# Performance work log

Hardware: AMD Instinct MI355X
Metric: run time of the kernel (lower is better)

The kernel has to match this reference:

```python
import jax, jax.numpy as jnp
import numpy as np

H = 8
DA, DP, DK = 2048, 1024, 1024
B, N = 4, 2048
DOUT = 512
INNER = (DA + DP + DK) // H  # 512 = heads*dim_head


def setup_inputs() -> dict:
    key = jax.random.key(0)
    ks = jax.random.split(key, 7)
    x = jax.random.normal(ks[0], (B, N, DA + DP + DK), jnp.float32)
    mask = jax.random.randint(ks[1], (B, 1, N, N), 0, 2, jnp.int32)
    W_a = jax.random.normal(ks[2], (3 * DA // H, DA), jnp.float32) * (DA ** -0.5)
    W_p = jax.random.normal(ks[3], (3 * DP // H, DP), jnp.float32) * (DP ** -0.5)
    W_k = jax.random.normal(ks[4], (3 * DK // H, DK), jnp.float32) * (DK ** -0.5)
    W_out = jax.random.normal(ks[5], (DOUT, INNER), jnp.float32) * (INNER ** -0.5)
    b_out = jnp.zeros((DOUT,), jnp.float32)
    return {"x": x, "W_a": W_a, "W_p": W_p, "W_k": W_k,
            "W_out": W_out, "b_out": b_out, "mask": mask}


def _heads(t):  # [b, n, h*d] -> [b, h, n, d]
    b, n, hd = t.shape
    return t.reshape(b, n, H, hd // H).transpose(0, 2, 1, 3)


def reference(x, W_a, W_p, W_k, W_out, b_out, mask):
    # three branch QKV projections (each branch sees its own slice of x)
    qkv_a = x[..., :DA] @ W_a.T                      # [b, n, 3*DA/H]
    qkv_p = x[..., DA:DA + DP] @ W_p.T               # [b, n, 3*DP/H]
    qkv_k = x[..., DA + DP:] @ W_k.T                 # [b, n, 3*DK/H]
    q_a, k_a, v_a = [_heads(t) for t in jnp.split(qkv_a, 3, axis=-1)]
    q_p, k_p, v_p = [_heads(t) for t in jnp.split(qkv_p, 3, axis=-1)]
    q_k, k_k, v_k = [_heads(t) for t in jnp.split(qkv_k, 3, axis=-1)]

    m = mask > 0                                     # [b, 1, n, n]
    neg = jnp.asarray(-1e10, x.dtype)

    def branch(q, k, d):
        dots = jnp.einsum('bhid,bhjd->bhij', q, k) * (d ** -0.5)
        return jax.nn.softmax(jnp.where(m, dots, neg), axis=-1)

    # betas = [1,1,1] normalized -> 1/3 each (the nn.Parameters are unused in fwd)
    attn = (branch(q_a, k_a, DA) + branch(q_p, k_p, DP) + branch(q_k, k_k, DK)) / 3.0

    v = jnp.concatenate([v_a, v_p, v_k], axis=-1)    # [b, h, n, INNER/H]
    out = jnp.einsum('bhij,bhjd->bhid', attn, v)     # [b, h, n, INNER/H]
    out = out.transpose(0, 2, 1, 3).reshape(x.shape[0], x.shape[1], INNER)
    return out @ W_out.T + b_out
```

## Files before the change

kernel.cpp:

```cpp
#include <hip/hip_runtime.h>
#include <hip/hip_bf16.h>

typedef __attribute__((ext_vector_type(8))) __bf16 bf16x8;
typedef __attribute__((ext_vector_type(4))) float f32x4;
typedef unsigned short u16;
typedef unsigned int u32;
typedef unsigned long long u64;

__device__ __forceinline__ u32 cvtpk(float lo, float hi) {
  u32 r;
  asm("v_cvt_pk_bf16_f32 %0, %1, %2" : "=v"(r) : "v"(lo), "v"(hi));
  return r;
}
__device__ __forceinline__ float rexp2(float x) {
  float r;
  asm("v_exp_f32 %0, %1" : "=v"(r) : "v"(x));
  return r;
}
__device__ __forceinline__ void gl_lds16(const void* g, void* l) {
  __builtin_amdgcn_global_load_lds((const __attribute__((address_space(1))) void*)g,
                                   (__attribute__((address_space(3))) void*)l, 16, 0, 0);
}

__global__ __launch_bounds__(256) void prep_kernel(
    const float* __restrict__ x, u16* __restrict__ xb,
    const float* __restrict__ Wa, const float* __restrict__ Wp,
    const float* __restrict__ Wk, const float* __restrict__ Wo,
    u16* __restrict__ Wab, u16* __restrict__ Wpb,
    u16* __restrict__ Wkb, u16* __restrict__ Wob,
    const int* __restrict__ mask, u64* __restrict__ bits, int xblocks) {
  int bid = blockIdx.x;
  if (bid < xblocks) {
    const int idx = (bid * 256 + threadIdx.x) * 16;
    const float4 a0 = *(const float4*)(x + idx);
    const float4 a1 = *(const float4*)(x + idx + 4);
    const float4 a2 = *(const float4*)(x + idx + 8);
    const float4 a3 = *(const float4*)(x + idx + 12);
    uint4 t0, t1;
    t0.x = cvtpk(a0.x, a0.y); t0.y = cvtpk(a0.z, a0.w);
    t0.z = cvtpk(a1.x, a1.y); t0.w = cvtpk(a1.z, a1.w);
    t1.x = cvtpk(a2.x, a2.y); t1.y = cvtpk(a2.z, a2.w);
    t1.z = cvtpk(a3.x, a3.y); t1.w = cvtpk(a3.z, a3.w);
    *(uint4*)(xb + idx) = t0;
    *(uint4*)(xb + idx + 8) = t1;
    return;
  }
  bid -= xblocks;
  if (bid < 2560) {
    const float* s; u16* d; int base;
    if (bid < 1536)      { s = Wa; d = Wab; base = bid; }
    else if (bid < 1920) { s = Wp; d = Wpb; base = bid - 1536; }
    else if (bid < 2304) { s = Wk; d = Wkb; base = bid - 1920; }
    else                 { s = Wo; d = Wob; base = bid - 2304; }
    const int idx = (base * 256 + threadIdx.x) * 4;
    const float4 v = *(const float4*)(s + idx);
    *(uint2*)(d + idx) = make_uint2(cvtpk(v.x, v.y), cvtpk(v.z, v.w));
    return;
  }
  bid -= 2560;
  const int lane = threadIdx.x & 63;
  const long long gw = (long long)bid * 4 + (threadIdx.x >> 6);
  const long long nwaves = 1024LL * 4;
  const long long nwords = 16777216LL / 64;
  for (long long i = gw; i < nwords; i += nwaves) {
    const int m = mask[i * 64 + lane];
    const u64 bal = __ballot(m > 0);
    if (lane == 0) bits[i] = bal;
  }
}

__device__ __forceinline__ void qkv_store(
    float v0, float v1, float v2, float v3, int m_base, int c,
    int dhs, int seg, float fs,
    u16* __restrict__ Qb, u16* __restrict__ Kb, u16* __restrict__ Vt) {
  const int which = c >> (3 + dhs);
  const float f = (which == 0) ? fs : 1.0f;
  const u32 r01 = cvtpk(v0 * f, v1 * f);
  const u32 r23 = cvtpk(v2 * f, v3 * f);
  const u16 bvv[4] = {(u16)r01, (u16)(r01 >> 16), (u16)r23, (u16)(r23 >> 16)};
  const int hd_mask = (8 << dhs) - 1;
  const int r = c & hd_mask;
  const int hh = r >> dhs;
  const int d = r & ((1 << dhs) - 1);
  #pragma unroll
  for (int j = 0; j < 4; ++j) {
    const int m = m_base + j;
    const int bb = m >> 11, n = m & 2047;
    const size_t bhn = (size_t)(bb * 8 + hh) * 2048 + n;
    const u16 bv = bvv[j];
    if (which == 0)      Qb[bhn * 64 + seg + d] = bv;
    else if (which == 1) Kb[bhn * 64 + seg + d] = bv;
    else {
      const int nk6 = n & 63;
      const int pos = ((nk6 >> 5) << 5) | (((nk6 & 15) >> 2) << 3)
                    | ((nk6 & 3) << 1) | ((nk6 >> 4) & 1);
      Vt[((size_t)(bb * 8 + hh) * 64 + seg + d) * 2048 + (n & ~63) + pos] = bv;
    }
  }
}

__global__ __launch_bounds__(256) void qkv_gemm_kernel(
    const u16* __restrict__ xb, const u16* __restrict__ Wa,
    const u16* __restrict__ Wp, const u16* __restrict__ Wk,
    u16* __restrict__ Qb, u16* __restrict__ Kb, u16* __restrict__ Vt) {
  __shared__ u16 lA[64 * 64];
  __shared__ u16 lB[128 * 64];

  const int tid = threadIdx.x;
  const int w = tid >> 6, l = tid & 63;
  const int lr = l & 15, lg = l >> 4;

  const int wg = blockIdx.x;
  const int xcd = wg & 7;
  const int q = wg >> 3;
  const int mtl = q / 12, nt = q % 12;
  const int mt = (xcd << 4) + mtl;

  const u16* W; int xoff, Kd, col0, dhs, seg;
  if (nt < 6)      { W = Wa; xoff = 0;    Kd = 2048; col0 = nt * 128;       dhs = 5; seg = 0;  }
  else if (nt < 9) { W = Wp; xoff = 2048; Kd = 1024; col0 = (nt - 6) * 128; dhs = 4; seg = 32; }
  else             { W = Wk; xoff = 3072; Kd = 1024; col0 = (nt - 9) * 128; dhs = 4; seg = 48; }
  const float qscale = (dhs == 5) ? 0.031880107f : 0.045084220f;

  const int m0 = mt * 64;
  f32x4 acc[4][2] = {};
  const int ubase = tid & ~63;

  const int nk = Kd >> 6;
  #pragma unroll 1
  for (int kt = 0; kt < nk; ++kt) {
    const int k0 = kt << 6;
    #pragma unroll
    for (int i = 0; i < 2; ++i) {
      const int ch = i * 256 + tid;
      const int row = ch >> 3, c8 = (ch & 7) << 3;
      gl_lds16(xb + (size_t)(m0 + row) * 4096 + xoff + k0 + c8,
               lA + (size_t)(i * 256 + ubase) * 8);
    }
    #pragma unroll
    for (int i = 0; i < 4; ++i) {
      const int ch = i * 256 + tid;
      const int row = ch >> 3, c8 = (ch & 7) << 3;
      gl_lds16(W + (size_t)(col0 + row) * Kd + k0 + c8,
               lB + (size_t)(i * 256 + ubase) * 8);
    }
    __syncthreads();
    bf16x8 af[4][2], bfr[2][2];
    #pragma unroll
    for (int mi = 0; mi < 4; ++mi) {
      af[mi][0] = *(const bf16x8*)(lA + (mi * 16 + lr) * 64 + lg * 8);
      af[mi][1] = *(const bf16x8*)(lA + (mi * 16 + lr) * 64 + 32 + lg * 8);
    }
    #pragma unroll
    for (int ni = 0; ni < 2; ++ni) {
      bfr[ni][0] = *(const bf16x8*)(lB + (w * 32 + ni * 16 + lr) * 64 + lg * 8);
      bfr[ni][1] = *(const bf16x8*)(lB + (w * 32 + ni * 16 + lr) * 64 + 32 + lg * 8);
    }
    #pragma unroll
    for (int mi = 0; mi < 4; ++mi)
      #pragma unroll
      for (int ni = 0; ni < 2; ++ni) {
        acc[mi][ni] = __builtin_amdgcn_mfma_f32_16x16x32_bf16(af[mi][0], bfr[ni][0], acc[mi][ni], 0, 0, 0);
        acc[mi][ni] = __builtin_amdgcn_mfma_f32_16x16x32_bf16(af[mi][1], bfr[ni][1], acc[mi][ni], 0, 0, 0);
      }
    __syncthreads();
  }

  #pragma unroll
  for (int mi = 0; mi < 4; ++mi)
    #pragma unroll
    for (int ni = 0; ni < 2; ++ni)
      qkv_store(acc[mi][ni][0], acc[mi][ni][1], acc[mi][ni][2], acc[mi][ni][3],
                m0 + mi * 16 + lg * 4, col0 + w * 32 + ni * 16 + lr,
                dhs, seg, qscale, Qb, Kb, Vt);
}

__global__ __launch_bounds__(256) void qkv_gemm_f32_kernel(
    const float* __restrict__ x, const u16* __restrict__ Wa,
    const u16* __restrict__ Wp, const u16* __restrict__ Wk,
    u16* __restrict__ Qb, u16* __restrict__ Kb, u16* __restrict__ Vt) {
  __shared__ u16 lA[128 * 64];
  __shared__ u16 lB[128 * 64];

  const int tid = threadIdx.x;
  const int w = tid >> 6, l = tid & 63;
  const int lr = l & 15, lg = l >> 4;
  const int wr = w >> 1, wc = w & 1;

  const int wg = blockIdx.x;
  const int xcd = wg & 7;
  const int q = wg >> 3;
  const int mtl = q / 12, nt = q % 12;
  const int mt = (xcd << 3) + mtl;

  const u16* W; int xoff, Kd, col0, dhs, seg;
  if (nt < 6)      { W = Wa; xoff = 0;    Kd = 2048; col0 = nt * 128;       dhs = 5; seg = 0;  }
  else if (nt < 9) { W = Wp; xoff = 2048; Kd = 1024; col0 = (nt - 6) * 128; dhs = 4; seg = 32; }
  else             { W = Wk; xoff = 3072; Kd = 1024; col0 = (nt - 9) * 128; dhs = 4; seg = 48; }
  const float qscale = (dhs == 5) ? 0.031880107f : 0.045084220f;

  const int m0 = mt * 128;
  f32x4 acc[4][4] = {};
  const int ubase = tid & ~63;

  const int nk = Kd >> 6;
  #pragma unroll 1
  for (int kt = 0; kt < nk; ++kt) {
    const int k0 = kt << 6;
    #pragma unroll
    for (int i = 0; i < 4; ++i) {
      const int ch = i * 256 + tid;
      const int row = ch >> 3, c8 = (ch & 7) << 3;
      const float* src = x + (size_t)(m0 + row) * 4096 + xoff + k0 + c8;
      const float4 a0 = *(const float4*)(src);
      const float4 a1 = *(const float4*)(src + 4);
      uint4 t;
      t.x = cvtpk(a0.x, a0.y); t.y = cvtpk(a0.z, a0.w);
      t.z = cvtpk(a1.x, a1.y); t.w = cvtpk(a1.z, a1.w);
      *(uint4*)(lA + (size_t)row * 64 + c8) = t;
    }
    #pragma unroll
    for (int i = 0; i < 4; ++i) {
      const int ch = i * 256 + tid;
      const int row = ch >> 3, c8 = (ch & 7) << 3;
      gl_lds16(W + (size_t)(col0 + row) * Kd + k0 + c8,
               lB + (size_t)(i * 256 + ubase) * 8);
    }
    __syncthreads();
    bf16x8 af[4][2], bfr[4][2];
    #pragma unroll
    for (int mi = 0; mi < 4; ++mi) {
      af[mi][0] = *(const bf16x8*)(lA + (wr * 64 + mi * 16 + lr) * 64 + lg * 8);
      af[mi][1] = *(const bf16x8*)(lA + (wr * 64 + mi * 16 + lr) * 64 + 32 + lg * 8);
    }
    #pragma unroll
    for (int ni = 0; ni < 4; ++ni) {
      bfr[ni][0] = *(const bf16x8*)(lB + (wc * 64 + ni * 16 + lr) * 64 + lg * 8);
      bfr[ni][1] = *(const bf16x8*)(lB + (wc * 64 + ni * 16 + lr) * 64 + 32 + lg * 8);
    }
    #pragma unroll
    for (int mi = 0; mi < 4; ++mi)
      #pragma unroll
      for (int ni = 0; ni < 4; ++ni) {
        acc[mi][ni] = __builtin_amdgcn_mfma_f32_16x16x32_bf16(af[mi][0], bfr[ni][0], acc[mi][ni], 0, 0, 0);
        acc[mi][ni] = __builtin_amdgcn_mfma_f32_16x16x32_bf16(af[mi][1], bfr[ni][1], acc[mi][ni], 0, 0, 0);
      }
    __syncthreads();
  }
  #pragma unroll
  for (int mi = 0; mi < 4; ++mi)
    #pragma unroll
    for (int ni = 0; ni < 4; ++ni)
      qkv_store(acc[mi][ni][0], acc[mi][ni][1], acc[mi][ni][2], acc[mi][ni][3],
                m0 + wr * 64 + mi * 16 + lg * 4, col0 + wc * 64 + ni * 16 + lr,
                dhs, seg, qscale, Qb, Kb, Vt);
}

__global__ __launch_bounds__(256) void attn_kernel(
    const u16* __restrict__ Qb, const u16* __restrict__ Kb,
    const u16* __restrict__ Vt, const u32* __restrict__ mbits,
    u16* __restrict__ aout) {
  struct SMem {
    u16 sK[2][64 * 64];
    u16 sV[2][64 * 64];
  };
  __shared__ SMem sm;

  const int tid = threadIdx.x;
  const int w = tid >> 6, l = tid & 63;
  const int lr = l & 15, lg = l >> 4;
  const int wg = blockIdx.x;
  const int xcd = wg & 7, rr0 = wg >> 3;
  const int bh = (xcd << 2) + (rr0 >> 5);
  const int qt = rr0 & 31;
  const int b = bh >> 3, h = bh & 7;
  const int q0 = qt << 6;
  const size_t bhN = (size_t)bh * 2048;
  const int ubase = tid & ~63;

  const u16* qrow = Qb + (bhN + q0 + w * 16 + lr) * 64;
  const bf16x8 qf_a  = *(const bf16x8*)(qrow + lg * 8);
  const bf16x8 qf_pk = *(const bf16x8*)(qrow + 32 + lg * 8);
  bf16x8 zero8 = {};
  const bf16x8 qf_p = (lg < 2) ? qf_pk : zero8;
  const bf16x8 qf_k = (lg < 2) ? zero8 : qf_pk;

  const u32* mptr = mbits + ((size_t)b * 2048 + q0 + w * 16 + lr) * 64;

  auto stageK = [&](int kt, int buf) {
    const int k0 = kt << 6;
    #pragma unroll
    for (int i = 0; i < 2; ++i) {
      const int p = i * 256 + tid;
      const int r = p >> 3, wd = p & 7;
      gl_lds16(Kb + (bhN + k0 + r) * 64 + (wd ^ (r & 7)) * 8,
               &sm.sK[buf][0] + (size_t)(i * 256 + ubase) * 8);
    }
  };
  auto stageV = [&](int kt, int buf) {
    const int k0 = kt << 6;
    #pragma unroll
    for (int i = 0; i < 2; ++i) {
      const int p = i * 256 + tid;
      const int r = p >> 3, wd = p & 7;
      gl_lds16(Vt + ((size_t)bh * 64 + r) * 2048 + k0 + (wd ^ (r & 7)) * 8,
               &sm.sV[buf][0] + (size_t)(i * 256 + ubase) * 8);
    }
  };

  stageK(0, 0); stageV(0, 0);

  bf16x8 vones;
  #pragma unroll
  for (int e = 0; e < 8; ++e) vones[e] = __builtin_bit_cast(__bf16, (u16)0x3F80);

  f32x4 oacc[3][4] = {};
  f32x4 osum[3] = {};
  const int c4 = (lg << 2);
  const int xk = lr & 7;

  #pragma unroll 1
  for (int kt = 0; kt < 32; ++kt) {
    const int cur = kt & 1;
    if (kt < 31) { stageK(kt + 1, cur ^ 1); stageV(kt + 1, cur ^ 1); }
    if (kt < 31) asm volatile("s_waitcnt vmcnt(4)" ::: "memory");
    else         asm volatile("s_waitcnt vmcnt(0)" ::: "memory");
    __builtin_amdgcn_sched_barrier(0);
    __builtin_amdgcn_s_barrier();

    const uint2 mk = *(const uint2*)(mptr + (kt << 1));
    u32 msk[4][2];
    #pragma unroll
    for (int j = 0; j < 4; ++j) {
      const int c = c4 + j;
      const u32 u0 = (mk.x >> c) & 0x00010001u;
      const u32 u1 = (mk.y >> c) & 0x00010001u;
      msk[j][0] = (u0 << 16) - u0;
      msk[j][1] = (u1 << 16) - u1;
    }

    bf16x8 vb[4][2];
    #pragma unroll
    for (int ct = 0; ct < 4; ++ct) {
      const u16* vrow = &sm.sV[cur][0] + (ct * 16 + lr) * 64;
      vb[ct][0] = *(const bf16x8*)(vrow + (lg ^ xk) * 8);
      vb[ct][1] = *(const bf16x8*)(vrow + ((lg + 4) ^ xk) * 8);
    }

    const f32x4 fz = {0.f, 0.f, 0.f, 0.f};
    auto softpv = [&](f32x4 (&sacc)[4], int s) {
      uint4 pw0, pw1;
      u32* w0 = (u32*)&pw0; u32* w1 = (u32*)&pw1;
      #pragma unroll
      for (int j = 0; j < 4; ++j) {
        w0[j] = cvtpk(rexp2(sacc[0][j]), rexp2(sacc[1][j])) & msk[j][0];
        w1[j] = cvtpk(rexp2(sacc[2][j]), rexp2(sacc[3][j])) & msk[j][1];
      }
      const bf16x8 pa0 = __builtin_bit_cast(bf16x8, pw0);
      const bf16x8 pa1 = __builtin_bit_cast(bf16x8, pw1);
      __builtin_amdgcn_s_setprio(1);
      #pragma unroll
      for (int ct = 0; ct < 4; ++ct) {
        oacc[s][ct] = __builtin_amdgcn_mfma_f32_16x16x32_bf16(pa0, vb[ct][0], oacc[s][ct], 0, 0, 0);
        oacc[s][ct] = __builtin_amdgcn_mfma_f32_16x16x32_bf16(pa1, vb[ct][1], oacc[s][ct], 0, 0, 0);
      }
      osum[s] = __builtin_amdgcn_mfma_f32_16x16x32_bf16(pa0, vones, osum[s], 0, 0, 0);
      osum[s] = __builtin_amdgcn_mfma_f32_16x16x32_bf16(pa1, vones, osum[s], 0, 0, 0);
      __builtin_amdgcn_s_setprio(0);
    };

    {
      f32x4 sacc[4];
      __builtin_amdgcn_s_setprio(1);
      #pragma unroll
      for (int t = 0; t < 4; ++t) {
        const bf16x8 kf = *(const bf16x8*)(&sm.sK[cur][0] + (t * 16 + lr) * 64 + ((lg ^ xk) * 8));
        sacc[t] = __builtin_amdgcn_mfma_f32_16x16x32_bf16(kf, qf_a, fz, 0, 0, 0);
      }
      __builtin_amdgcn_s_setprio(0);
      softpv(sacc, 0);
    }
    {
      f32x4 sacc[4];
      __builtin_amdgcn_s_setprio(1);
      #pragma unroll
      for (int t = 0; t < 4; ++t) {
        const bf16x8 kf = *(const bf16x8*)(&sm.sK[cur][0] + (t * 16 + lr) * 64 + (((lg + 4) ^ xk) * 8));
        sacc[t] = __builtin_amdgcn_mfma_f32_16x16x32_bf16(kf, qf_p, fz, 0, 0, 0);
      }
      __builtin_amdgcn_s_setprio(0);
      softpv(sacc, 1);
    }
    {
      f32x4 sacc[4];
      __builtin_amdgcn_s_setprio(1);
      #pragma unroll
      for (int t = 0; t < 4; ++t) {
        const bf16x8 kf = *(const bf16x8*)(&sm.sK[cur][0] + (t * 16 + lr) * 64 + (((lg + 4) ^ xk) * 8));
        sacc[t] = __builtin_amdgcn_mfma_f32_16x16x32_bf16(kf, qf_k, fz, 0, 0, 0);
      }
      __builtin_amdgcn_s_setprio(0);
      softpv(sacc, 2);
    }

    __builtin_amdgcn_s_barrier();
  }

  float linv[3][4];
  #pragma unroll
  for (int s = 0; s < 3; ++s)
    #pragma unroll
    for (int j = 0; j < 4; ++j)
      linv[s][j] = 1.0f / (3.0f * osum[s][j] + 1e-30f);

  #pragma unroll
  for (int ct = 0; ct < 4; ++ct) {
    float vj[4];
    #pragma unroll
    for (int j = 0; j < 4; ++j)
      vj[j] = oacc[0][ct][j] * linv[0][j]
            + oacc[1][ct][j] * linv[1][j]
            + oacc[2][ct][j] * linv[2][j];
    const u32 r01 = cvtpk(vj[0], vj[1]);
    const u32 r23 = cvtpk(vj[2], vj[3]);
    const u16 bvv[4] = {(u16)r01, (u16)(r01 >> 16), (u16)r23, (u16)(r23 >> 16)};
    #pragma unroll
    for (int j = 0; j < 4; ++j) {
      const int row = q0 + w * 16 + lg * 4 + j;
      const int col = h * 64 + ct * 16 + lr;
      aout[((size_t)b * 2048 + row) * 512 + col] = bvv[j];
    }
  }
}

__global__ __launch_bounds__(256) void out_gemm_kernel(
    const u16* __restrict__ A, const u16* __restrict__ Wo,
    const float* __restrict__ bias, float* __restrict__ out) {
  __shared__ u16 lA[64 * 64];
  __shared__ u16 lB[64 * 64];

  const int tid = threadIdx.x;
  const int w = tid >> 6, l = tid & 63;
  const int lr = l & 15, lg = l >> 4;

  const int wg = blockIdx.x;
  const int xcd = wg & 7;
  const int q = wg >> 3;
  const int mt = (xcd << 4) + (q >> 3);
  const int nt = q & 7;
  const int col0 = nt * 64;
  const int m0 = mt * 64;
  f32x4 acc[4] = {};
  const int ubase = tid & ~63;

  #pragma unroll 1
  for (int kt = 0; kt < 8; ++kt) {
    const int k0 = kt << 6;
    #pragma unroll
    for (int i = 0; i < 2; ++i) {
      const int ch = i * 256 + tid;
      const int row = ch >> 3, c8 = (ch & 7) << 3;
      gl_lds16(A + (size_t)(m0 + row) * 512 + k0 + c8, lA + (size_t)(i * 256 + ubase) * 8);
    }
    #pragma unroll
    for (int i = 0; i < 2; ++i) {
      const int ch = i * 256 + tid;
      const int row = ch >> 3, c8 = (ch & 7) << 3;
      gl_lds16(Wo + (size_t)(col0 + row) * 512 + k0 + c8, lB + (size_t)(i * 256 + ubase) * 8);
    }
    __syncthreads();
    bf16x8 af[4][2], bfr[2];
    #pragma unroll
    for (int mi = 0; mi < 4; ++mi) {
      af[mi][0] = *(const bf16x8*)(lA + (mi * 16 + lr) * 64 + lg * 8);
      af[mi][1] = *(const bf16x8*)(lA + (mi * 16 + lr) * 64 + 32 + lg * 8);
    }
    bfr[0] = *(const bf16x8*)(lB + (w * 16 + lr) * 64 + lg * 8);
    bfr[1] = *(const bf16x8*)(lB + (w * 16 + lr) * 64 + 32 + lg * 8);
    #pragma unroll
    for (int mi = 0; mi < 4; ++mi) {
      acc[mi] = __builtin_amdgcn_mfma_f32_16x16x32_bf16(af[mi][0], bfr[0], acc[mi], 0, 0, 0);
      acc[mi] = __builtin_amdgcn_mfma_f32_16x16x32_bf16(af[mi][1], bfr[1], acc[mi], 0, 0, 0);
    }
    __syncthreads();
  }

  const int c = col0 + w * 16 + lr;
  const float bv = bias[c];
  #pragma unroll
  for (int mi = 0; mi < 4; ++mi)
    #pragma unroll
    for (int j = 0; j < 4; ++j) {
      const int m = m0 + mi * 16 + lg * 4 + j;
      out[(size_t)m * 512 + c] = acc[mi][j] + bv;
    }
}

extern "C" void kernel_launch(void* const* d_in, const int* in_sizes, int n_in,
                              void* d_out, int out_size, void* d_ws, size_t ws_size,
                              hipStream_t stream) {
  const float* x    = (const float*)d_in[0];
  const float* Wa   = (const float*)d_in[1];
  const float* Wp   = (const float*)d_in[2];
  const float* Wk   = (const float*)d_in[3];
  const float* Wo   = (const float*)d_in[4];
  const float* bo   = (const float*)d_in[5];
  const int* mask   = (const int*)d_in[6];
  float* out = (float*)d_out;

  char* ws = (char*)d_ws;
  u16* Wab = (u16*)ws;
  u16* Wpb = (u16*)(ws + 3145728);
  u16* Wkb = (u16*)(ws + 3932160);
  u16* Wob = (u16*)(ws + 4718592);
  u16* Qb  = (u16*)(ws + 5242880);
  u16* Kb  = (u16*)(ws + 13631488);
  u16* Vt  = (u16*)(ws + 22020096);
  u64* Mb  = (u64*)(ws + 30408704);
  u16* Ao  = (u16*)(ws + 32505856);
  u16* xb  = (u16*)(ws + 40894464);

  const bool use_xb = ws_size >= (size_t)40894464 + 67108864;
  const int xblocks = use_xb ? 8192 : 0;

  prep_kernel<<<xblocks + 2560 + 1024, 256, 0, stream>>>(
      x, xb, Wa, Wp, Wk, Wo, Wab, Wpb, Wkb, Wob, mask, (u64*)Mb, xblocks);
  if (use_xb) {
    qkv_gemm_kernel<<<1536, 256, 0, stream>>>(xb, Wab, Wpb, Wkb, Qb, Kb, Vt);
  } else {
    qkv_gemm_f32_kernel<<<768, 256, 0, stream>>>(x, Wab, Wpb, Wkb, Qb, Kb, Vt);
  }
  attn_kernel<<<1024, 256, 0, stream>>>(Qb, Kb, Vt, (const u32*)Mb, Ao);
  out_gemm_kernel<<<1024, 256, 0, stream>>>(Ao, Wob, bo, out);
}
```

Before: 284.3 us.

## Use 512-thread attention blocks covering 128 query rows to share K/V tiles

The attention kernel now runs 8 waves per block over 128 query rows instead of 4 waves over 64, so each staged 64-key K/V tile in LDS serves twice as many queries. This halves the global K/V traffic and the number of blocks. Each thread now issues one async global-to-LDS load per tensor per tile, with precomputed pointers. The loop is unrolled by two so the double-buffer index is a compile-time constant. In exchange there are fewer blocks, larger barriers, and more register pressure under the 512-thread launch bound.

```diff
diff --git a/kernel.cpp b/kernel.cpp
--- a/kernel.cpp
+++ b/kernel.cpp
@@ -256,7 +256,7 @@
                 dhs, seg, qscale, Qb, Kb, Vt);
 }
 
-__global__ __launch_bounds__(256) void attn_kernel(
+__global__ __launch_bounds__(512) void attn_kernel(
     const u16* __restrict__ Qb, const u16* __restrict__ Kb,
     const u16* __restrict__ Vt, const u32* __restrict__ mbits,
     u16* __restrict__ aout) {
@@ -271,10 +271,10 @@
   const int lr = l & 15, lg = l >> 4;
   const int wg = blockIdx.x;
   const int xcd = wg & 7, rr0 = wg >> 3;
-  const int bh = (xcd << 2) + (rr0 >> 5);
-  const int qt = rr0 & 31;
+  const int bh = (xcd << 2) + (rr0 >> 4);
+  const int qt = rr0 & 15;
   const int b = bh >> 3, h = bh & 7;
-  const int q0 = qt << 6;
+  const int q0 = qt << 7;
   const size_t bhN = (size_t)bh * 2048;
   const int ubase = tid & ~63;
 
@@ -287,28 +287,14 @@
 
   const u32* mptr = mbits + ((size_t)b * 2048 + q0 + w * 16 + lr) * 64;
 
-  auto stageK = [&](int kt, int buf) {
-    const int k0 = kt << 6;
-    #pragma unroll
-    for (int i = 0; i < 2; ++i) {
-      const int p = i * 256 + tid;
-      const int r = p >> 3, wd = p & 7;
-      gl_lds16(Kb + (bhN + k0 + r) * 64 + (wd ^ (r & 7)) * 8,
-               &sm.sK[buf][0] + (size_t)(i * 256 + ubase) * 8);
-    }
-  };
-  auto stageV = [&](int kt, int buf) {
-    const int k0 = kt << 6;
-    #pragma unroll
-    for (int i = 0; i < 2; ++i) {
-      const int p = i * 256 + tid;
-      const int r = p >> 3, wd = p & 7;
-      gl_lds16(Vt + ((size_t)bh * 64 + r) * 2048 + k0 + (wd ^ (r & 7)) * 8,
-               &sm.sV[buf][0] + (size_t)(i * 256 + ubase) * 8);
-    }
-  };
-
-  stageK(0, 0); stageV(0, 0);
+  const int sr = tid >> 3, swd = tid & 7;
+  const u16* kp = Kb + (bhN + sr) * 64 + (swd ^ (sr & 7)) * 8;
+  const u16* vp = Vt + ((size_t)bh * 64 + sr) * 2048 + (swd ^ (sr & 7)) * 8;
+  u16* dK[2] = { &sm.sK[0][0] + ubase * 8, &sm.sK[1][0] + ubase * 8 };
+  u16* dV[2] = { &sm.sV[0][0] + ubase * 8, &sm.sV[1][0] + ubase * 8 };
+
+  gl_lds16(kp, dK[0]);
+  gl_lds16(vp, dV[0]);
 
   bf16x8 vones;
   #pragma unroll
@@ -319,12 +305,14 @@
   const int c4 = (lg << 2);
   const int xk = lr & 7;
 
-  #pragma unroll 1
-  for (int kt = 0; kt < 32; ++kt) {
-    const int cur = kt & 1;
-    if (kt < 31) { stageK(kt + 1, cur ^ 1); stageV(kt + 1, cur ^ 1); }
-    if (kt < 31) asm volatile("s_waitcnt vmcnt(4)" ::: "memory");
-    else         asm volatile("s_waitcnt vmcnt(0)" ::: "memory");
+  auto body = [&](int kt, int cur, bool st) {
+    if (st) {
+      gl_lds16(kp + (size_t)(kt + 1) * 4096, dK[cur ^ 1]);
+      gl_lds16(vp + (size_t)(kt + 1) * 64, dV[cur ^ 1]);
+      asm volatile("s_waitcnt vmcnt(2)" ::: "memory");
+    } else {
+      asm volatile("s_waitcnt vmcnt(0)" ::: "memory");
+    }
     __builtin_amdgcn_sched_barrier(0);
     __builtin_amdgcn_s_barrier();
 
@@ -404,6 +392,12 @@
     }
 
     __builtin_amdgcn_s_barrier();
+  };
+
+  #pragma unroll 1
+  for (int it = 0; it < 16; ++it) {
+    body(2 * it, 0, true);
+    body(2 * it + 1, 1, it < 15);
   }
 
   float linv[3][4];
@@ -530,6 +524,6 @@
   } else {
     qkv_gemm_f32_kernel<<<768, 256, 0, stream>>>(x, Wab, Wpb, Wkb, Qb, Kb, Vt);
   }
-  attn_kernel<<<1024, 256, 0, stream>>>(Qb, Kb, Vt, (const u32*)Mb, Ao);
+  attn_kernel<<<512, 512, 0, stream>>>(Qb, Kb, Vt, (const u32*)Mb, Ao);
   out_gemm_kernel<<<1024, 256, 0, stream>>>(Ao, Wob, bo, out);
 }
```

After: 289.9 us. No clear change (+1.9%).
